# Kernel optimization log

Measured on AMD Instinct MI355X. Metric: run time of the kernel, lower is better.

## Reference

```python
import jax, jax.numpy as jnp
import numpy as np

B, T, C = 2, 2048, 1024
N_HEAD = 16
G_NON = 32   # qgroup_size_non (layernorm / residual path)
G_LIN = 32   # qgroup_size_lin (linear path)
QMAX = 127.0
EPS = 1e-5


def quantize(x, G):
    """Group-wise symmetric int8 quantization along the last dim.
    Returns q (int8, same shape as x) and scales s with shape x.shape[:-1] + (D//G,)."""
    shp = x.shape
    xg = x.reshape(shp[:-1] + (shp[-1] // G, G))
    s = jnp.maximum(jnp.max(jnp.abs(xg), axis=-1) / QMAX, 1e-8)
    q = jnp.clip(jnp.round(xg / s[..., None]), -QMAX, QMAX).astype(jnp.int8)
    return q.reshape(shp), s


def dequant(q, s, G):
    shp = q.shape
    xg = q.astype(jnp.float32).reshape(shp[:-1] + (shp[-1] // G, G)) * s[..., None]
    return xg.reshape(shp)


def quant_dequant(x, G):
    """Fake-quantize (straight-through): forward = dequant(quantize(x))."""
    q, s = quantize(x, G)
    xd = dequant(q, s, G)
    return x + jax.lax.stop_gradient(xd - x)


def setup_inputs() -> dict:
    key = jax.random.key(0)
    k1, k2, k3, k4 = jax.random.split(key, 4)
    x = jax.random.normal(k1, (B, T, C), dtype=jnp.float32)
    # LN stats of x, produced by the previous block's int8_add_..._MeanVar
    mean = jnp.mean(x, axis=-1)
    rstd = 1.0 / jnp.sqrt(jnp.var(x, axis=-1) + EPS)
    qx, sx = quantize(x, G_NON)
    ln_w = 1.0 + 0.02 * jax.random.normal(k2, (C,), dtype=jnp.float32)
    w1 = 0.02 * jax.random.normal(k3, (3 * C, C), dtype=jnp.float32)   # c_attn.weight [out,in]
    w2 = 0.02 * jax.random.normal(k4, (C, C), dtype=jnp.float32)       # c_proj.weight [out,in]
    return {"x": x, "qx": qx.astype(jnp.int32), "sx": sx, "mean": mean,
            "rstd": rstd, "ln_w": ln_w, "w1": w1, "w2": w2}


def reference(x, qx, sx, mean, rstd, ln_w, w1, w2):
    hd = C // N_HEAD
    # ---- Part1: int8 layernorm (uses provided mean/rstd) + int8 c_attn linear ----
    ln_in = dequant(qx.astype(jnp.int8), sx, G_NON)               # [B,T,C]
    h = (ln_in - mean[..., None]) * rstd[..., None] * ln_w        # layernorm output
    hq = quant_dequant(h, G_NON)                                  # requantize activations
    w1q = quant_dequant(w1, G_LIN)                                # int8 weight
    qkv = jnp.einsum('btc,oc->bto', hq, w1q)                      # [B,T,3C]
    q, k, v = jnp.split(qkv, 3, axis=-1)
    q = q.reshape(B, T, N_HEAD, hd).transpose(0, 2, 1, 3)         # [B,H,T,hd]
    k = k.reshape(B, T, N_HEAD, hd).transpose(0, 2, 1, 3)
    v = v.reshape(B, T, N_HEAD, hd).transpose(0, 2, 1, 3)
    # ---- causal SDPA ----
    scores = jnp.einsum('bhqd,bhkd->bhqk', q, k) / jnp.sqrt(jnp.float32(hd))
    causal = jnp.tril(jnp.ones((T, T), dtype=bool))
    scores = jnp.where(causal, scores, jnp.float32(-1e30))
    attn = jax.nn.softmax(scores, axis=-1)
    y = jnp.einsum('bhqk,bhkd->bhqd', attn, v)
    y = y.transpose(0, 2, 1, 3).reshape(B, T, C)
    # ---- Part2: int8 c_proj linear + residual add with mean/var ----
    yq = quant_dequant(y, G_LIN)
    w2q = quant_dequant(w2, G_LIN)
    proj = jnp.einsum('btc,oc->bto', yq, w2q)
    fpx = x + proj                                                # fp residual output
    mean_o = jnp.mean(fpx, axis=-1)
    rstd_o = 1.0 / jnp.sqrt(jnp.var(fpx, axis=-1) + EPS)
    qo, so = quantize(fpx, G_NON)                                 # quantized output for next block
    return (fpx, qo, so, mean_o, rstd_o)
```

## Files before the change

### kernel.cpp

```cpp
#include <hip/hip_runtime.h>
#include <stdint.h>

#define BB 2
#define TT 2048
#define CC 1024
#define NH 16
#define HD 64
#define NG 32
#define ROWS (BB*TT)
#define C3 (3*CC)

typedef _Float16 half_t;
typedef __attribute__((ext_vector_type(8))) _Float16 half8;
typedef __attribute__((ext_vector_type(2))) __fp16 fp16x2;
typedef __attribute__((ext_vector_type(4))) float f32x4;

#define GLDS16(g, l) __builtin_amdgcn_global_load_lds( \
    (__attribute__((address_space(1))) void*)(g), \
    (__attribute__((address_space(3))) void*)(l), 16, 0, 0)

#define LOG2E 1.44269504f
#define DEFER_THR 5.5451774f

__device__ __forceinline__ uint32_t pk_h2(float a, float b) {
  union { fp16x2 h; uint32_t u; } cv;
  cv.h = __builtin_amdgcn_cvt_pkrtz(a, b);
  return cv.u;
}

__global__ void k_qdq_w(const float* __restrict__ w1, const float* __restrict__ w2,
                        half_t* __restrict__ o1, half_t* __restrict__ o2) {
  int g = blockIdx.x * blockDim.x + threadIdx.x;
  const float* src; half_t* dst; int gl;
  if (g < C3 * NG) { src = w1; dst = o1; gl = g; }
  else             { src = w2; dst = o2; gl = g - C3 * NG; }
  const float4* p = reinterpret_cast<const float4*>(src + (size_t)gl * 32);
  float v[32]; float amax = 0.f;
  #pragma unroll
  for (int i = 0; i < 8; ++i) {
    float4 t = p[i];
    v[4*i] = t.x; v[4*i+1] = t.y; v[4*i+2] = t.z; v[4*i+3] = t.w;
    amax = fmaxf(amax, fmaxf(fmaxf(fabsf(t.x), fabsf(t.y)), fmaxf(fabsf(t.z), fabsf(t.w))));
  }
  float s = fmaxf(amax / 127.0f, 1e-8f);
  half_t* o = dst + (size_t)gl * 32;
  #pragma unroll
  for (int c = 0; c < 4; ++c) {
    half8 ov;
    #pragma unroll
    for (int jj = 0; jj < 8; ++jj) {
      float q = fminf(fmaxf(rintf(v[c*8+jj] / s), -127.f), 127.f);
      ov[jj] = (half_t)(q * s);
    }
    *reinterpret_cast<half8*>(o + c*8) = ov;
  }
}

__global__ void k_qh(const int* __restrict__ qx, const float* __restrict__ sx,
                     const float* __restrict__ mean, const float* __restrict__ rstd,
                     const float* __restrict__ lnw, half_t* __restrict__ h16) {
  int g = blockIdx.x * blockDim.x + threadIdx.x;
  if (g >= ROWS * NG) return;
  int row = g >> 5, grp = g & 31;
  float sxv = sx[g];
  float mu = mean[row], rs = rstd[row];
  const int4* qp = reinterpret_cast<const int4*>(qx + (size_t)row * CC + grp * 32);
  const float4* wp = reinterpret_cast<const float4*>(lnw + grp * 32);
  float v[32]; float amax = 0.f;
  #pragma unroll
  for (int i = 0; i < 8; ++i) {
    int4 qv = qp[i]; float4 wv = wp[i];
    float h0 = ((float)qv.x * sxv - mu) * rs * wv.x;
    float h1 = ((float)qv.y * sxv - mu) * rs * wv.y;
    float h2 = ((float)qv.z * sxv - mu) * rs * wv.z;
    float h3 = ((float)qv.w * sxv - mu) * rs * wv.w;
    v[4*i] = h0; v[4*i+1] = h1; v[4*i+2] = h2; v[4*i+3] = h3;
    amax = fmaxf(amax, fmaxf(fmaxf(fabsf(h0), fabsf(h1)), fmaxf(fabsf(h2), fabsf(h3))));
  }
  float s = fmaxf(amax / 127.0f, 1e-8f);
  half_t* o = h16 + (size_t)row * CC + grp * 32;
  #pragma unroll
  for (int c = 0; c < 4; ++c) {
    half8 ov;
    #pragma unroll
    for (int jj = 0; jj < 8; ++jj) {
      float q = fminf(fmaxf(rintf(v[c*8+jj] / s), -127.f), 127.f);
      ov[jj] = (half_t)(q * s);
    }
    *reinterpret_cast<half8*>(o + c*8) = ov;
  }
}

template<typename TO>
__global__ __launch_bounds__(256) void k_gemm16(const half_t* __restrict__ A,
                                                const half_t* __restrict__ B,
                                                TO* __restrict__ Out, int N) {
  __shared__ __align__(16) half_t As[2*128*32];
  __shared__ __align__(16) half_t Bs[2*128*32];
  const int tid = threadIdx.x;
  const int wave = tid >> 6, lane = tid & 63;
  const int l15 = lane & 15, lg = lane >> 4;
  const int m0 = blockIdx.y * 128, n0 = blockIdx.x * 128;
  const int wm = (wave >> 1) * 64, wn = (wave & 1) * 64;
  f32x4 acc[4][4];
  #pragma unroll
  for (int i = 0; i < 4; ++i)
    #pragma unroll
    for (int jj = 0; jj < 4; ++jj) acc[i][jj] = f32x4{0.f, 0.f, 0.f, 0.f};
  const int srow = lane >> 2;
  const int scol = (lane & 3) * 8;
  for (int k0 = 0; k0 < 1024; k0 += 64) {
    #pragma unroll
    for (int s = 0; s < 4; ++s) {
      const int chunk = wave * 4 + s;
      const int panel = chunk >> 3, rg = chunk & 7;
      GLDS16(A + (size_t)(m0 + rg*16 + srow) * 1024 + k0 + panel*32 + scol,
             As + panel*4096 + rg*512);
      GLDS16(B + (size_t)(n0 + rg*16 + srow) * 1024 + k0 + panel*32 + scol,
             Bs + panel*4096 + rg*512);
    }
    __syncthreads();
    #pragma unroll
    for (int p = 0; p < 2; ++p) {
      half8 af[4], bf[4];
      #pragma unroll
      for (int i = 0; i < 4; ++i) {
        af[i] = *reinterpret_cast<const half8*>(As + p*4096 + (wm + i*16 + l15)*32 + lg*8);
        bf[i] = *reinterpret_cast<const half8*>(Bs + p*4096 + (wn + i*16 + l15)*32 + lg*8);
      }
      #pragma unroll
      for (int mi = 0; mi < 4; ++mi)
        #pragma unroll
        for (int ni = 0; ni < 4; ++ni)
          acc[mi][ni] = __builtin_amdgcn_mfma_f32_16x16x32_f16(af[mi], bf[ni], acc[mi][ni], 0, 0, 0);
    }
    __syncthreads();
  }
  const int crow = m0 + wm + lg * 4;
  const int ccol = n0 + wn + l15;
  #pragma unroll
  for (int mi = 0; mi < 4; ++mi)
    #pragma unroll
    for (int ni = 0; ni < 4; ++ni)
      #pragma unroll
      for (int r = 0; r < 4; ++r)
        Out[(size_t)(crow + mi*16 + r) * N + ccol + ni*16] = (TO)acc[mi][ni][r];
}

__global__ __launch_bounds__(512, 4) void k_attn16(const half_t* __restrict__ qkv,
                                                   half_t* __restrict__ y16) {
  __shared__ __align__(16) half_t Ks[2][64*72];
  __shared__ __align__(16) half_t Vt[2][64*72];
  __shared__ __align__(16) half_t Ps[8][16*72];
  const int tid = threadIdx.x;
  const int wave = tid >> 6, lane = tid & 63;
  const int l15 = lane & 15, lg = lane >> 4;
  const int w4 = wave & 3;
  const int bh = blockIdx.x, b = bh >> 4, h = bh & 15;
  const int j = blockIdx.y;
  const int qtB = 31 - j;
  const int qt = (wave >> 2) ? qtB : j;

  const size_t row = (size_t)(b * TT + qt * 64 + w4 * 16 + l15);
  const half_t* qp = qkv + row * C3 + h * HD + lg * 8;
  const half8 q0 = *reinterpret_cast<const half8*>(qp)      * (half_t)0.125f;
  const half8 q1 = *reinterpret_cast<const half8*>(qp + 32) * (half_t)0.125f;

  float m = -3.0e38f;
  f32x4 yacc[4];
  f32x4 lacc = f32x4{0,0,0,0};
  #pragma unroll
  for (int n = 0; n < 4; ++n) yacc[n] = f32x4{0,0,0,0};

  const int sj = tid >> 3, sc = (tid & 7) * 8;
  const int vkp = tid >> 4, vd0 = (tid & 15) * 4;
  const int vxor = ((vd0 >> 3) & 7) << 2;
  const int pxor = (l15 & 3) << 3;
  half_t* pw = &Ps[wave][0];

  int vdw0[4], vdw1[4];
  #pragma unroll
  for (int n = 0; n < 4; ++n) {
    const int d = n*16 + l15;
    const int x = ((n*2 + (l15 >> 3)) & 7) << 2;
    vdw0[n] = (d*36 + lg*4) ^ x;
    vdw1[n] = (d*36 + 16 + lg*4) ^ x;
  }

  half8 ones8;
  #pragma unroll
  for (int i = 0; i < 8; ++i) ones8[i] = (half_t)1.0f;

  half8 k0r; uint2 u0r, u1r;
  const half_t* kvb = qkv + ((size_t)b * TT) * C3 + CC + h * HD;
  auto kload = [&](int kt) {
    const half_t* kp = kvb + (size_t)(kt*64 + sj) * C3 + sc;
    k0r = *reinterpret_cast<const half8*>(kp);
    const half_t* vp = kvb + (size_t)(kt*64 + vkp*2) * C3 + CC + vd0;
    u0r = *reinterpret_cast<const uint2*>(vp);
    u1r = *reinterpret_cast<const uint2*>(vp + C3);
  };
  auto stage = [&](int buf) {
    *reinterpret_cast<half8*>(&Ks[buf][0] + sj*72 + sc) = k0r;
    uint32_t* vt32 = reinterpret_cast<uint32_t*>(&Vt[buf][0]);
    vt32[((vd0+0)*36 + vkp) ^ vxor] = __builtin_amdgcn_perm(u1r.x, u0r.x, 0x05040100u);
    vt32[((vd0+1)*36 + vkp) ^ vxor] = __builtin_amdgcn_perm(u1r.x, u0r.x, 0x07060302u);
    vt32[((vd0+2)*36 + vkp) ^ vxor] = __builtin_amdgcn_perm(u1r.y, u0r.y, 0x05040100u);
    vt32[((vd0+3)*36 + vkp) ^ vxor] = __builtin_amdgcn_perm(u1r.y, u0r.y, 0x07060302u);
  };

  kload(0);
  stage(0);
  kload(1);
  __syncthreads();
  for (int kt = 0; kt <= qtB; ++kt) {
    const int cur = kt & 1;
    if (kt < qtB) {
      stage(cur ^ 1);
      if (kt + 2 <= qtB) kload(kt + 2);
    }
    if (kt <= qt) {
      const half_t* ksb = &Ks[cur][0];
      const uint32_t* vt32 = reinterpret_cast<const uint32_t*>(&Vt[cur][0]);
      f32x4 sacc[4];
      __builtin_amdgcn_s_setprio(1);
      #pragma unroll
      for (int kg = 0; kg < 4; ++kg) {
        const half8 a0 = *reinterpret_cast<const half8*>(ksb + (kg*16 + l15)*72 + lg*8);
        const half8 a1 = *reinterpret_cast<const half8*>(ksb + (kg*16 + l15)*72 + lg*8 + 32);
        f32x4 t = f32x4{0,0,0,0};
        t = __builtin_amdgcn_mfma_f32_16x16x32_f16(a0, q0, t, 0, 0, 0);
        t = __builtin_amdgcn_mfma_f32_16x16x32_f16(a1, q1, t, 0, 0, 0);
        sacc[kg] = t;
      }
      __builtin_amdgcn_s_setprio(0);
      float sv[16]; float tm = -3.0e38f;
      const bool diag = (kt == qt);
      #pragma unroll
      for (int kg = 0; kg < 4; ++kg)
        #pragma unroll
        for (int r = 0; r < 4; ++r) {
          float s = sacc[kg][r];
          if (diag && (kg*16 + lg*4 + r > w4*16 + l15)) s = -1e30f;
          sv[kg*4 + r] = s;
          tm = fmaxf(tm, s);
        }
      tm = fmaxf(tm, __shfl_xor(tm, 16));
      tm = fmaxf(tm, __shfl_xor(tm, 32));
      if (!__all(tm <= m + DEFER_THR)) {
        const float mn = fmaxf(m, tm);
        const float alpha = __builtin_amdgcn_exp2f((m - mn) * LOG2E);
        #pragma unroll
        for (int n = 0; n < 4; ++n) yacc[n] *= alpha;
        lacc *= alpha;
        m = mn;
      }
      const float nm = -m * LOG2E;
      #pragma unroll
      for (int i = 0; i < 16; ++i)
        sv[i] = __builtin_amdgcn_exp2f(fmaf(sv[i], LOG2E, nm));
      uint32_t* prow = reinterpret_cast<uint32_t*>(pw) + l15*36;
      #pragma unroll
      for (int kg = 0; kg < 4; ++kg) {
        uint2 pr;
        pr.x = pk_h2(sv[kg*4 + 0], sv[kg*4 + 1]);
        pr.y = pk_h2(sv[kg*4 + 2], sv[kg*4 + 3]);
        *reinterpret_cast<uint2*>(prow + ((kg*8 + lg*2) ^ pxor)) = pr;
      }
      __builtin_amdgcn_sched_barrier(0);
      const half8 pb0 = *reinterpret_cast<const half8*>(
          pw + (l15*36 + ((lg*4) ^ pxor)) * 2);
      const half8 pb1 = *reinterpret_cast<const half8*>(
          pw + (l15*36 + ((16 + lg*4) ^ pxor)) * 2);
      __builtin_amdgcn_s_setprio(1);
      #pragma unroll
      for (int n = 0; n < 4; ++n) {
        const half8 va0 = *reinterpret_cast<const half8*>(vt32 + vdw0[n]);
        const half8 va1 = *reinterpret_cast<const half8*>(vt32 + vdw1[n]);
        yacc[n] = __builtin_amdgcn_mfma_f32_16x16x32_f16(va0, pb0, yacc[n], 0, 0, 0);
        yacc[n] = __builtin_amdgcn_mfma_f32_16x16x32_f16(va1, pb1, yacc[n], 0, 0, 0);
      }
      lacc = __builtin_amdgcn_mfma_f32_16x16x32_f16(ones8, pb0, lacc, 0, 0, 0);
      lacc = __builtin_amdgcn_mfma_f32_16x16x32_f16(ones8, pb1, lacc, 0, 0, 0);
      __builtin_amdgcn_s_setprio(0);
    }
    __syncthreads();
  }

  const float inv = 1.0f / lacc[0];
  float v[16];
  #pragma unroll
  for (int n = 0; n < 4; ++n)
    #pragma unroll
    for (int r = 0; r < 4; ++r) v[n*4 + r] = yacc[n][r] * inv;
  half_t* yp = y16 + row * CC + h * HD;
  #pragma unroll
  for (int g = 0; g < 2; ++g) {
    float am = 0.f;
    #pragma unroll
    for (int t = 0; t < 8; ++t) am = fmaxf(am, fabsf(v[g*8 + t]));
    am = fmaxf(am, __shfl_xor(am, 16));
    am = fmaxf(am, __shfl_xor(am, 32));
    const float s = fmaxf(am / 127.0f, 1e-8f);
    const float qi = 1.0f / s;
    #pragma unroll
    for (int nn = 0; nn < 2; ++nn) {
      const int n = g*2 + nn;
      union { half_t h4[4]; uint64_t u; } pk;
      #pragma unroll
      for (int r = 0; r < 4; ++r) {
        float q = fminf(fmaxf(rintf(v[n*4 + r] * qi), -127.f), 127.f);
        pk.h4[r] = (half_t)(q * s);
      }
      *reinterpret_cast<uint64_t*>(yp + n*16 + lg*4) = pk.u;
    }
  }
}

__global__ __launch_bounds__(256) void k_final(
    const float* __restrict__ x, const half_t* __restrict__ proj,
    float* __restrict__ out_fpx, float* __restrict__ out_qo, float* __restrict__ out_so,
    float* __restrict__ out_mean, float* __restrict__ out_rstd) {
  __shared__ float red[16];
  int row = blockIdx.x;
  int tid = threadIdx.x;
  size_t base = (size_t)row * CC + tid * 4;
  float4 xv = *reinterpret_cast<const float4*>(x + base);
  union { uint64_t u; half_t h[4]; } pp;
  pp.u = *reinterpret_cast<const uint64_t*>(proj + base);
  float4 f;
  f.x = xv.x + (float)pp.h[0]; f.y = xv.y + (float)pp.h[1];
  f.z = xv.z + (float)pp.h[2]; f.w = xv.w + (float)pp.h[3];
  *reinterpret_cast<float4*>(out_fpx + base) = f;
  float sum = f.x + f.y + f.z + f.w;
  float sq  = f.x*f.x + f.y*f.y + f.z*f.z + f.w*f.w;
  #pragma unroll
  for (int off = 1; off < 64; off <<= 1) {
    sum += __shfl_xor(sum, off);
    sq  += __shfl_xor(sq, off);
  }
  int wid = tid >> 6, lane = tid & 63;
  if (lane == 0) { red[wid] = sum; red[8 + wid] = sq; }
  __syncthreads();
  if (tid == 0) {
    float s4 = red[0] + red[1] + red[2] + red[3];
    float q4 = red[8] + red[9] + red[10] + red[11];
    float mu = s4 * (1.0f / CC);
    float var = q4 * (1.0f / CC) - mu * mu;
    out_mean[row] = mu;
    out_rstd[row] = 1.0f / sqrtf(var + 1e-5f);
  }
  float amax = fmaxf(fmaxf(fabsf(f.x), fabsf(f.y)), fmaxf(fabsf(f.z), fabsf(f.w)));
  #pragma unroll
  for (int off = 1; off < 8; off <<= 1) amax = fmaxf(amax, __shfl_xor(amax, off, 8));
  float s = fmaxf(amax / 127.0f, 1e-8f);
  int g = tid >> 3, li = tid & 7;
  if (li == 0) out_so[row * NG + g] = s;
  float4 qo;
  qo.x = fminf(fmaxf(rintf(f.x / s), -127.f), 127.f);
  qo.y = fminf(fmaxf(rintf(f.y / s), -127.f), 127.f);
  qo.z = fminf(fmaxf(rintf(f.z / s), -127.f), 127.f);
  qo.w = fminf(fmaxf(rintf(f.w / s), -127.f), 127.f);
  *reinterpret_cast<float4*>(out_qo + base) = qo;
}

extern "C" void kernel_launch(void* const* d_in, const int* in_sizes, int n_in,
                              void* d_out, int out_size, void* d_ws, size_t ws_size,
                              hipStream_t stream) {
  const float* x    = (const float*)d_in[0];
  const int*   qx   = (const int*)d_in[1];
  const float* sx   = (const float*)d_in[2];
  const float* mean = (const float*)d_in[3];
  const float* rstd = (const float*)d_in[4];
  const float* lnw  = (const float*)d_in[5];
  const float* w1   = (const float*)d_in[6];
  const float* w2   = (const float*)d_in[7];

  float* out = (float*)d_out;
  float* o_fpx  = out;
  float* o_qo   = o_fpx + (size_t)ROWS * CC;
  float* o_so   = o_qo  + (size_t)ROWS * CC;
  float* o_mean = o_so  + (size_t)ROWS * NG;
  float* o_rstd = o_mean + ROWS;

  size_t off = 0;
  char* wsb = (char*)d_ws;
  auto alloc = [&](size_t bytes) -> void* {
    void* p = wsb + off;
    off += (bytes + 255) & ~(size_t)255;
    return p;
  };
  half_t* h16   = (half_t*)alloc((size_t)ROWS * CC * 2);
  half_t* w116  = (half_t*)alloc((size_t)C3 * CC * 2);
  half_t* w216  = (half_t*)alloc((size_t)CC * CC * 2);
  half_t* qkv16 = (half_t*)alloc((size_t)ROWS * C3 * 2);
  half_t* y16   = (half_t*)alloc((size_t)ROWS * CC * 2);
  half_t* proj  = (half_t*)alloc((size_t)ROWS * CC * 2);

  k_qdq_w<<<(C3 * NG + CC * NG) / 256, 256, 0, stream>>>(w1, w2, w116, w216);
  k_qh<<<(ROWS * NG) / 256, 256, 0, stream>>>(qx, sx, mean, rstd, lnw, h16);
  k_gemm16<half_t><<<dim3(C3 / 128, ROWS / 128), 256, 0, stream>>>(h16, w116, qkv16, C3);
  k_attn16<<<dim3(BB * NH, 16), 512, 0, stream>>>(qkv16, y16);
  k_gemm16<half_t><<<dim3(CC / 128, ROWS / 128), 256, 0, stream>>>(y16, w216, proj, CC);
  k_final<<<ROWS, 256, 0, stream>>>(x, proj, o_fpx, o_qo, o_so, o_mean, o_rstd);
}
```

Before: 135.5 us.

## Split-K proj GEMM, XCD-aware block swizzle, and smaller K-step tiles

The c_proj GEMM now splits K into two halves over blockIdx.z, writing two half-precision partial outputs that k_final sums with the residual. This doubles the block count for the small 256-block GEMM to fill more CUs. Both GEMMs also remap block indices with a modulo-8 swizzle so neighbouring tiles land on the same XCD. The K step per iteration drops from 64 to 32, halving LDS use at the cost of twice as many barriers. The extra partial buffer adds memory traffic, and summing two fp16 partials adds some rounding.

```diff
diff --git a/kernel.cpp b/kernel.cpp
--- a/kernel.cpp
+++ b/kernel.cpp
@@ -94,13 +94,18 @@
 template<typename TO>
 __global__ __launch_bounds__(256) void k_gemm16(const half_t* __restrict__ A,
                                                 const half_t* __restrict__ B,
-                                                TO* __restrict__ Out, int N) {
-  __shared__ __align__(16) half_t As[2*128*32];
-  __shared__ __align__(16) half_t Bs[2*128*32];
+                                                TO* __restrict__ Out, int N,
+                                                int gx, int cpx, int klen) {
+  __shared__ __align__(16) half_t As[128*32];
+  __shared__ __align__(16) half_t Bs[128*32];
   const int tid = threadIdx.x;
   const int wave = tid >> 6, lane = tid & 63;
   const int l15 = lane & 15, lg = lane >> 4;
-  const int m0 = blockIdx.y * 128, n0 = blockIdx.x * 128;
+  const int flat = blockIdx.y * gx + blockIdx.x;
+  const int swz = (flat & 7) * cpx + (flat >> 3);
+  const int m0 = (swz / gx) * 128, n0 = (swz % gx) * 128;
+  const int kbeg = blockIdx.z * klen;
+  TO* out = Out + (size_t)blockIdx.z * ROWS * N;
   const int wm = (wave >> 1) * 64, wn = (wave & 1) * 64;
   f32x4 acc[4][4];
   #pragma unroll
@@ -109,31 +114,26 @@
     for (int jj = 0; jj < 4; ++jj) acc[i][jj] = f32x4{0.f, 0.f, 0.f, 0.f};
   const int srow = lane >> 2;
   const int scol = (lane & 3) * 8;
-  for (int k0 = 0; k0 < 1024; k0 += 64) {
-    #pragma unroll
-    for (int s = 0; s < 4; ++s) {
-      const int chunk = wave * 4 + s;
-      const int panel = chunk >> 3, rg = chunk & 7;
-      GLDS16(A + (size_t)(m0 + rg*16 + srow) * 1024 + k0 + panel*32 + scol,
-             As + panel*4096 + rg*512);
-      GLDS16(B + (size_t)(n0 + rg*16 + srow) * 1024 + k0 + panel*32 + scol,
-             Bs + panel*4096 + rg*512);
+  const int seg0 = wave * 2;
+  for (int k0 = kbeg; k0 < kbeg + klen; k0 += 32) {
+    #pragma unroll
+    for (int s = 0; s < 2; ++s) {
+      const int seg = seg0 + s;
+      GLDS16(A + (size_t)(m0 + seg*16 + srow) * 1024 + k0 + scol, As + seg*512);
+      GLDS16(B + (size_t)(n0 + seg*16 + srow) * 1024 + k0 + scol, Bs + seg*512);
     }
     __syncthreads();
-    #pragma unroll
-    for (int p = 0; p < 2; ++p) {
-      half8 af[4], bf[4];
-      #pragma unroll
-      for (int i = 0; i < 4; ++i) {
-        af[i] = *reinterpret_cast<const half8*>(As + p*4096 + (wm + i*16 + l15)*32 + lg*8);
-        bf[i] = *reinterpret_cast<const half8*>(Bs + p*4096 + (wn + i*16 + l15)*32 + lg*8);
-      }
-      #pragma unroll
-      for (int mi = 0; mi < 4; ++mi)
-        #pragma unroll
-        for (int ni = 0; ni < 4; ++ni)
-          acc[mi][ni] = __builtin_amdgcn_mfma_f32_16x16x32_f16(af[mi], bf[ni], acc[mi][ni], 0, 0, 0);
-    }
+    half8 af[4], bf[4];
+    #pragma unroll
+    for (int i = 0; i < 4; ++i) {
+      af[i] = *reinterpret_cast<const half8*>(As + (wm + i*16 + l15)*32 + lg*8);
+      bf[i] = *reinterpret_cast<const half8*>(Bs + (wn + i*16 + l15)*32 + lg*8);
+    }
+    #pragma unroll
+    for (int mi = 0; mi < 4; ++mi)
+      #pragma unroll
+      for (int ni = 0; ni < 4; ++ni)
+        acc[mi][ni] = __builtin_amdgcn_mfma_f32_16x16x32_f16(af[mi], bf[ni], acc[mi][ni], 0, 0, 0);
     __syncthreads();
   }
   const int crow = m0 + wm + lg * 4;
@@ -144,7 +144,7 @@
     for (int ni = 0; ni < 4; ++ni)
       #pragma unroll
       for (int r = 0; r < 4; ++r)
-        Out[(size_t)(crow + mi*16 + r) * N + ccol + ni*16] = (TO)acc[mi][ni][r];
+        out[(size_t)(crow + mi*16 + r) * N + ccol + ni*16] = (TO)acc[mi][ni][r];
 }
 
 __global__ __launch_bounds__(512, 4) void k_attn16(const half_t* __restrict__ qkv,
@@ -318,7 +318,8 @@
 }
 
 __global__ __launch_bounds__(256) void k_final(
-    const float* __restrict__ x, const half_t* __restrict__ proj,
+    const float* __restrict__ x, const half_t* __restrict__ p0,
+    const half_t* __restrict__ p1,
     float* __restrict__ out_fpx, float* __restrict__ out_qo, float* __restrict__ out_so,
     float* __restrict__ out_mean, float* __restrict__ out_rstd) {
   __shared__ float red[16];
@@ -326,11 +327,14 @@
   int tid = threadIdx.x;
   size_t base = (size_t)row * CC + tid * 4;
   float4 xv = *reinterpret_cast<const float4*>(x + base);
-  union { uint64_t u; half_t h[4]; } pp;
-  pp.u = *reinterpret_cast<const uint64_t*>(proj + base);
+  union { uint64_t u; half_t h[4]; } pa, pb;
+  pa.u = *reinterpret_cast<const uint64_t*>(p0 + base);
+  pb.u = *reinterpret_cast<const uint64_t*>(p1 + base);
   float4 f;
-  f.x = xv.x + (float)pp.h[0]; f.y = xv.y + (float)pp.h[1];
-  f.z = xv.z + (float)pp.h[2]; f.w = xv.w + (float)pp.h[3];
+  f.x = xv.x + (float)pa.h[0] + (float)pb.h[0];
+  f.y = xv.y + (float)pa.h[1] + (float)pb.h[1];
+  f.z = xv.z + (float)pa.h[2] + (float)pb.h[2];
+  f.w = xv.w + (float)pa.h[3] + (float)pb.h[3];
   *reinterpret_cast<float4*>(out_fpx + base) = f;
   float sum = f.x + f.y + f.z + f.w;
   float sq  = f.x*f.x + f.y*f.y + f.z*f.z + f.w*f.w;
@@ -395,12 +399,15 @@
   half_t* w216  = (half_t*)alloc((size_t)CC * CC * 2);
   half_t* qkv16 = (half_t*)alloc((size_t)ROWS * C3 * 2);
   half_t* y16   = (half_t*)alloc((size_t)ROWS * CC * 2);
-  half_t* proj  = (half_t*)alloc((size_t)ROWS * CC * 2);
+  half_t* proj  = (half_t*)alloc((size_t)2 * ROWS * CC * 2);
 
   k_qdq_w<<<(C3 * NG + CC * NG) / 256, 256, 0, stream>>>(w1, w2, w116, w216);
   k_qh<<<(ROWS * NG) / 256, 256, 0, stream>>>(qx, sx, mean, rstd, lnw, h16);
-  k_gemm16<half_t><<<dim3(C3 / 128, ROWS / 128), 256, 0, stream>>>(h16, w116, qkv16, C3);
+  k_gemm16<half_t><<<dim3(C3 / 128, ROWS / 128, 1), 256, 0, stream>>>(
+      h16, w116, qkv16, C3, C3 / 128, (C3 / 128) * (ROWS / 128) / 8, 1024);
   k_attn16<<<dim3(BB * NH, 16), 512, 0, stream>>>(qkv16, y16);
-  k_gemm16<half_t><<<dim3(CC / 128, ROWS / 128), 256, 0, stream>>>(y16, w216, proj, CC);
-  k_final<<<ROWS, 256, 0, stream>>>(x, proj, o_fpx, o_qo, o_so, o_mean, o_rstd);
-}
+  k_gemm16<half_t><<<dim3(CC / 128, ROWS / 128, 2), 256, 0, stream>>>(
+      y16, w216, proj, CC, CC / 128, (CC / 128) * (ROWS / 128) / 8, 512);
+  k_final<<<ROWS, 256, 0, stream>>>(x, proj, proj + (size_t)ROWS * CC,
+                                    o_fpx, o_qo, o_so, o_mean, o_rstd);
+}
```

New measurement: 132.5 us. 1.02x faster.
